# Performance work log

Hardware: AMD Instinct MI355X
Metric: run time of the kernel (lower is better)

## Reference

```python
import jax, jax.numpy as jnp
import numpy as np


def setup_inputs() -> dict:
    key = jax.random.key(0)
    k1, k2 = jax.random.split(key)
    B, N, M = 16, 4096, 4096
    xyz1 = jax.random.normal(k1, (B, N, 3), dtype=jnp.float32)
    xyz2 = jax.random.normal(k2, (B, M, 3), dtype=jnp.float32)
    return {"xyz1": xyz1, "xyz2": xyz2}


def reference(xyz1, xyz2):
    sq1 = jnp.sum(xyz1 * xyz1, axis=-1)            # [B, N]
    sq2 = jnp.sum(xyz2 * xyz2, axis=-1)            # [B, M]
    inner = jnp.einsum('bnd,bmd->bnm', xyz1, xyz2)  # [B, N, M]
    d = sq1[:, :, None] + sq2[:, None, :] - 2.0 * inner
    dist1 = jnp.min(d, axis=2)  # nearest in xyz2 for each point of xyz1, [B, N]
    dist2 = jnp.min(d, axis=1)  # nearest in xyz1 for each point of xyz2, [B, M]
    return (jnp.mean(dist1), jnp.mean(dist2))
```

## Files before the change

kernel.cpp:

```cpp
#include <hip/hip_runtime.h>
#include <float.h>

#define BATCH  16
#define NPTS   4096
#define TOTALP (BATCH * NPTS)
#define NQ     (2 * TOTALP)

typedef _Float16 half8  __attribute__((ext_vector_type(8)));
typedef float    f32x16 __attribute__((ext_vector_type(16)));

#define ONE2 0x3C003C00u

__device__ __forceinline__ unsigned enc(float f)
{
    unsigned b = __float_as_uint(f);
    return (b & 0x80000000u) ? ~b : (b | 0x80000000u);
}
__device__ __forceinline__ float dec(unsigned k)
{
    return (k & 0x80000000u) ? __uint_as_float(k & 0x7FFFFFFFu)
                             : __uint_as_float(~k);
}

__device__ __forceinline__ unsigned pk(_Float16 lo, _Float16 hi)
{
    const unsigned a = (unsigned)__builtin_bit_cast(unsigned short, lo);
    const unsigned b = (unsigned)__builtin_bit_cast(unsigned short, hi);
    return a | (b << 16);
}

__device__ __forceinline__ float min16(const f32x16& d, float acc)
{
    const float m1 = fminf(fminf(d[0],  d[1]),  d[2]);
    const float m2 = fminf(fminf(d[3],  d[4]),  d[5]);
    const float m3 = fminf(fminf(d[6],  d[7]),  d[8]);
    const float m4 = fminf(fminf(d[9],  d[10]), d[11]);
    const float m5 = fminf(fminf(d[12], d[13]), d[14]);
    const float m6 = fminf(fminf(m1, m2), m3);
    const float m7 = fminf(fminf(m4, m5), d[15]);
    return fminf(fminf(m6, m7), acc);
}

__global__ __launch_bounds__(256) void prep_kernel(
    const float* __restrict__ xyz1, const float* __restrict__ xyz2,
    uint4* __restrict__ packQ, uint4* __restrict__ packO)
{
    const int i = blockIdx.x * 256 + threadIdx.x;
    const float* src = (i < TOTALP) ? xyz1 : xyz2;
    const int p = i & (TOTALP - 1);
    const float x = src[3 * p + 0];
    const float y = src[3 * p + 1];
    const float z = src[3 * p + 2];
    const float sq = x * x + y * y + z * z;
    const _Float16 sh = (_Float16)sq;
    const _Float16 sl = (_Float16)(sq - (float)sh);

    const _Float16 vxh = (_Float16)x, vyh = (_Float16)y, vzh = (_Float16)z;
    const _Float16 vxl = (_Float16)(x - (float)vxh);
    const _Float16 vyl = (_Float16)(y - (float)vyh);
    const _Float16 vzl = (_Float16)(z - (float)vzh);
    packO[i] = make_uint4(pk(vxh, vyh), pk(vzh, vxl), pk(vyl, vzl), pk(sh, sl));

    const float ux = -2.0f * x, uy = -2.0f * y, uz = -2.0f * z;
    const _Float16 uxh = (_Float16)ux, uyh = (_Float16)uy, uzh = (_Float16)uz;
    const _Float16 uxl = (_Float16)(ux - (float)uxh);
    const _Float16 uyl = (_Float16)(uy - (float)uyh);
    const _Float16 uzl = (_Float16)(uz - (float)uzh);
    packQ[i] = make_uint4(pk(uxh, uyh), pk(uzh, uxl), pk(uyl, uzl), pk(sh, sl));
}

__global__ __launch_bounds__(256) void chamfer_flip(
    const uint4* __restrict__ packQ, const uint4* __restrict__ packO,
    unsigned* __restrict__ keys)
{
    __shared__ uint4 Ast[2][512];

    const int blk = blockIdx.x;
    const int ch  = blk & 3;
    const int qc  = (blk >> 2) & 7;
    const int b   = (blk >> 5) & 15;
    const int dir = blk >> 9;

    const int lane = threadIdx.x & 63;
    const int wv   = threadIdx.x >> 6;
    const int n32  = lane & 31;
    const int half = lane >> 5;

    const int qbase = dir * TOTALP + b * NPTS + qc * 512 + wv * 128;
    half8 bfrag[4];
#pragma unroll
    for (int qf = 0; qf < 4; ++qf) {
        const uint4 d = packQ[qbase + qf * 32 + n32];
        const uint4 u = half ? make_uint4(d.y, d.z, d.w, ONE2)
                             : make_uint4(d.x, d.y, d.z, d.x);
        bfrag[qf] = __builtin_bit_cast(half8, u);
    }

    float acc[4];
#pragma unroll
    for (int qf = 0; qf < 4; ++qf) acc[qf] = FLT_MAX;

    f32x16 cz;
#pragma unroll
    for (int r = 0; r < 16; ++r) cz[r] = 0.0f;

    const int obase = (dir ^ 1) * TOTALP + b * NPTS + ch * 1024;

    for (int round = 0; round < 2; ++round) {
        __syncthreads();
        for (int r = threadIdx.x; r < 512; r += 256) {
            const uint4 d = packO[obase + round * 512 + r];
            uint4 h0, h1;
            h0.x = d.x;
            h0.y = (d.y & 0xFFFFu) | (d.x << 16);
            h0.z = (d.x >> 16) | (d.y << 16);
            h0.w = (d.y >> 16) | (d.z << 16);
            h1.x = (d.z >> 16) | (d.y & 0xFFFF0000u);
            h1.y = d.z;
            h1.z = ONE2;
            h1.w = d.w;
            Ast[0][r] = h0;
            Ast[1][r] = h1;
        }
        __syncthreads();

        for (int tile = 0; tile < 16; ++tile) {
            const half8 af = __builtin_bit_cast(
                half8, Ast[half][tile * 32 + n32]);
#pragma unroll
            for (int qf = 0; qf < 4; ++qf) {
                const f32x16 dd = __builtin_amdgcn_mfma_f32_32x32x16_f16(
                    af, bfrag[qf], cz, 0, 0, 0);
                acc[qf] = min16(dd, acc[qf]);
            }
        }
    }

#pragma unroll
    for (int qf = 0; qf < 4; ++qf) {
        float v = acc[qf];
        v = fminf(v, __shfl_xor(v, 32));
        if (lane < 32)
            atomicMin(&keys[qbase + qf * 32 + n32], enc(v));
    }
}

__global__ __launch_bounds__(256) void chamfer_final_atomic(
    const unsigned* __restrict__ keys, float* __restrict__ out)
{
    const int dir = blockIdx.x >> 8;
    const int qi  = ((blockIdx.x & 255) << 8) + threadIdx.x;
    const int q   = (dir << 16) + qi;

    float d = dec(keys[q]);

    for (int off = 32; off > 0; off >>= 1)
        d += __shfl_down(d, off);

    __shared__ float wsum[4];
    const int lane = threadIdx.x & 63;
    const int wv   = threadIdx.x >> 6;
    if (lane == 0) wsum[wv] = d;
    __syncthreads();
    if (threadIdx.x == 0) {
        float s = wsum[0] + wsum[1] + wsum[2] + wsum[3];
        atomicAdd(&out[dir], s * (1.0f / (float)TOTALP));
    }
}

__global__ void zero_out_kernel(float* __restrict__ out)
{
    if (threadIdx.x == 0) { out[0] = 0.0f; out[1] = 0.0f; }
}

__global__ __launch_bounds__(256) void chamfer_raw_kernel(
    const float* __restrict__ xyz1, const float* __restrict__ xyz2,
    float* __restrict__ out)
{
    const int blk = blockIdx.x;
    const int dir = blk >> 8;
    const int idx = blk & 255;
    const int b   = idx >> 4;
    const int n0  = (idx & 15) << 8;

    const float* __restrict__ own = (dir == 0 ? xyz1 : xyz2) + (size_t)b * NPTS * 3;
    const float* __restrict__ opp = (dir == 0 ? xyz2 : xyz1) + (size_t)b * NPTS * 3;

    const int n = n0 + threadIdx.x;
    const float ax = own[3 * n + 0];
    const float ay = own[3 * n + 1];
    const float az = own[3 * n + 2];

    float best = FLT_MAX;
    for (int m = 0; m < NPTS; m += 4) {
#pragma unroll
        for (int u = 0; u < 4; ++u) {
            const float px = opp[3 * (m + u) + 0];
            const float py = opp[3 * (m + u) + 1];
            const float pz = opp[3 * (m + u) + 2];
            const float dx = px - ax, dy = py - ay, dz = pz - az;
            float d = dx * dx;
            d = fmaf(dy, dy, d);
            d = fmaf(dz, dz, d);
            best = fminf(best, d);
        }
    }

    float d = best;
    for (int off = 32; off > 0; off >>= 1)
        d += __shfl_down(d, off);

    __shared__ float wsum[4];
    const int lane = threadIdx.x & 63;
    const int wv   = threadIdx.x >> 6;
    if (lane == 0) wsum[wv] = d;
    __syncthreads();
    if (threadIdx.x == 0) {
        float s = wsum[0] + wsum[1] + wsum[2] + wsum[3];
        atomicAdd(&out[dir], s * (1.0f / (float)TOTALP));
    }
}

extern "C" void kernel_launch(void* const* d_in, const int* in_sizes, int n_in,
                              void* d_out, int out_size, void* d_ws, size_t ws_size,
                              hipStream_t stream)
{
    const float* xyz1 = (const float*)d_in[0];
    const float* xyz2 = (const float*)d_in[1];
    float* out = (float*)d_out;

    const size_t keys_bytes = (size_t)NQ * sizeof(unsigned);
    const size_t pack_bytes = (size_t)NQ * sizeof(uint4);

    if (ws_size >= keys_bytes + 2 * pack_bytes) {
        unsigned* keys  = (unsigned*)d_ws;
        uint4*    packQ = (uint4*)((char*)d_ws + keys_bytes);
        uint4*    packO = (uint4*)((char*)d_ws + keys_bytes + pack_bytes);

        hipMemsetAsync(keys, 0xFF, keys_bytes, stream);
        hipMemsetAsync(out, 0, 2 * sizeof(float), stream);
        prep_kernel<<<NQ / 256, 256, 0, stream>>>(xyz1, xyz2, packQ, packO);
        chamfer_flip<<<1024, 256, 0, stream>>>(packQ, packO, keys);
        chamfer_final_atomic<<<NQ / 256, 256, 0, stream>>>(keys, out);
    } else {
        zero_out_kernel<<<1, 64, 0, stream>>>(out);
        chamfer_raw_kernel<<<512, 256, 0, stream>>>(xyz1, xyz2, out);
    }
}
```

Baseline: 95.51 us.

## Pre-build MFMA A-operand planes, stream from global, fold memsets into prep

The prep kernel now writes the two half-precision A-fragment layouts directly into two global planes, so the main kernel no longer stages and reshuffles opposite points through LDS with barriers. Each wave loads its A fragment straight from global with one-tile-ahead prefetch. Work is split into 2048 blocks of 512 opposite points instead of 1024 blocks of 1024. The key and output memsets are folded into the prep kernel, which saves two API launches but issues more atomics and doubles the plane footprint.

Measured after the change: 94.31 us. Within noise of the previous version (-1.3%).

```diff
diff --git a/kernel.cpp b/kernel.cpp
--- a/kernel.cpp
+++ b/kernel.cpp
@@ -43,9 +43,13 @@
 
 __global__ __launch_bounds__(256) void prep_kernel(
     const float* __restrict__ xyz1, const float* __restrict__ xyz2,
-    uint4* __restrict__ packQ, uint4* __restrict__ packO)
+    uint4* __restrict__ packQ, uint4* __restrict__ planes,
+    unsigned* __restrict__ keys, float* __restrict__ out)
 {
     const int i = blockIdx.x * 256 + threadIdx.x;
+    if (i == 0) { out[0] = 0.0f; out[1] = 0.0f; }
+    keys[i] = 0xFFFFFFFFu;
+
     const float* src = (i < TOTALP) ? xyz1 : xyz2;
     const int p = i & (TOTALP - 1);
     const float x = src[3 * p + 0];
@@ -59,7 +63,10 @@
     const _Float16 vxl = (_Float16)(x - (float)vxh);
     const _Float16 vyl = (_Float16)(y - (float)vyh);
     const _Float16 vzl = (_Float16)(z - (float)vzh);
-    packO[i] = make_uint4(pk(vxh, vyh), pk(vzh, vxl), pk(vyl, vzl), pk(sh, sl));
+    planes[i]      = make_uint4(pk(vxh, vyh), pk(vzh, vxh),
+                                pk(vyh, vzh), pk(vxl, vyl));
+    planes[NQ + i] = make_uint4(pk(vzl, vxl), pk(vyl, vzl),
+                                ONE2,         pk(sh, sl));
 
     const float ux = -2.0f * x, uy = -2.0f * y, uz = -2.0f * z;
     const _Float16 uxh = (_Float16)ux, uyh = (_Float16)uy, uzh = (_Float16)uz;
@@ -69,17 +76,15 @@
     packQ[i] = make_uint4(pk(uxh, uyh), pk(uzh, uxl), pk(uyl, uzl), pk(sh, sl));
 }
 
-__global__ __launch_bounds__(256) void chamfer_flip(
-    const uint4* __restrict__ packQ, const uint4* __restrict__ packO,
+__global__ __launch_bounds__(256) void chamfer_flip2(
+    const uint4* __restrict__ packQ, const uint4* __restrict__ planes,
     unsigned* __restrict__ keys)
 {
-    __shared__ uint4 Ast[2][512];
-
     const int blk = blockIdx.x;
-    const int ch  = blk & 3;
-    const int qc  = (blk >> 2) & 7;
-    const int b   = (blk >> 5) & 15;
-    const int dir = blk >> 9;
+    const int ch  = blk & 7;
+    const int qc  = (blk >> 3) & 7;
+    const int b   = (blk >> 6) & 15;
+    const int dir = blk >> 10;
 
     const int lane = threadIdx.x & 63;
     const int wv   = threadIdx.x >> 6;
@@ -104,36 +109,20 @@
 #pragma unroll
     for (int r = 0; r < 16; ++r) cz[r] = 0.0f;
 
-    const int obase = (dir ^ 1) * TOTALP + b * NPTS + ch * 1024;
-
-    for (int round = 0; round < 2; ++round) {
-        __syncthreads();
-        for (int r = threadIdx.x; r < 512; r += 256) {
-            const uint4 d = packO[obase + round * 512 + r];
-            uint4 h0, h1;
-            h0.x = d.x;
-            h0.y = (d.y & 0xFFFFu) | (d.x << 16);
-            h0.z = (d.x >> 16) | (d.y << 16);
-            h0.w = (d.y >> 16) | (d.z << 16);
-            h1.x = (d.z >> 16) | (d.y & 0xFFFF0000u);
-            h1.y = d.z;
-            h1.z = ONE2;
-            h1.w = d.w;
-            Ast[0][r] = h0;
-            Ast[1][r] = h1;
+    const uint4* __restrict__ ap =
+        planes + (size_t)half * NQ + (dir ^ 1) * TOTALP + b * NPTS + ch * 512;
+
+    uint4 cur = ap[n32];
+    for (int tile = 0; tile < 16; ++tile) {
+        const uint4 nxt = ap[(((tile + 1) & 15) * 32) + n32];
+        const half8 af = __builtin_bit_cast(half8, cur);
+#pragma unroll
+        for (int qf = 0; qf < 4; ++qf) {
+            const f32x16 dd = __builtin_amdgcn_mfma_f32_32x32x16_f16(
+                af, bfrag[qf], cz, 0, 0, 0);
+            acc[qf] = min16(dd, acc[qf]);
         }
-        __syncthreads();
-
-        for (int tile = 0; tile < 16; ++tile) {
-            const half8 af = __builtin_bit_cast(
-                half8, Ast[half][tile * 32 + n32]);
-#pragma unroll
-            for (int qf = 0; qf < 4; ++qf) {
-                const f32x16 dd = __builtin_amdgcn_mfma_f32_32x32x16_f16(
-                    af, bfrag[qf], cz, 0, 0, 0);
-                acc[qf] = min16(dd, acc[qf]);
-            }
-        }
+        cur = nxt;
     }
 
 #pragma unroll
@@ -229,18 +218,17 @@
     const float* xyz2 = (const float*)d_in[1];
     float* out = (float*)d_out;
 
-    const size_t keys_bytes = (size_t)NQ * sizeof(unsigned);
-    const size_t pack_bytes = (size_t)NQ * sizeof(uint4);
-
-    if (ws_size >= keys_bytes + 2 * pack_bytes) {
-        unsigned* keys  = (unsigned*)d_ws;
-        uint4*    packQ = (uint4*)((char*)d_ws + keys_bytes);
-        uint4*    packO = (uint4*)((char*)d_ws + keys_bytes + pack_bytes);
-
-        hipMemsetAsync(keys, 0xFF, keys_bytes, stream);
-        hipMemsetAsync(out, 0, 2 * sizeof(float), stream);
-        prep_kernel<<<NQ / 256, 256, 0, stream>>>(xyz1, xyz2, packQ, packO);
-        chamfer_flip<<<1024, 256, 0, stream>>>(packQ, packO, keys);
+    const size_t keys_bytes  = (size_t)NQ * sizeof(unsigned);
+    const size_t packQ_bytes = (size_t)NQ * sizeof(uint4);
+    const size_t plane_bytes = (size_t)2 * NQ * sizeof(uint4);
+
+    if (ws_size >= keys_bytes + packQ_bytes + plane_bytes) {
+        unsigned* keys   = (unsigned*)d_ws;
+        uint4*    packQ  = (uint4*)((char*)d_ws + keys_bytes);
+        uint4*    planes = (uint4*)((char*)d_ws + keys_bytes + packQ_bytes);
+
+        prep_kernel<<<NQ / 256, 256, 0, stream>>>(xyz1, xyz2, packQ, planes, keys, out);
+        chamfer_flip2<<<2048, 256, 0, stream>>>(packQ, planes, keys);
         chamfer_final_atomic<<<NQ / 256, 256, 0, stream>>>(keys, out);
     } else {
         zero_out_kernel<<<1, 64, 0, stream>>>(out);
```
